# Kernel tuning notes

Hardware: AMD Instinct MI355X
Metric: run time of the kernel (lower is better)

Reference implementation:

```python
import jax, jax.numpy as jnp
import numpy as np

RETURN_SHAPE = (128, 128)


def dht2(x):
    # Discrete Hartley Transform over the spatial axes (2, 3):
    # H = Re(FFT) - Im(FFT). Unnormalized, matching scipy.fft default.
    f = jnp.fft.fftn(x, axes=(2, 3))
    return f.real - f.imag


def setup_inputs() -> dict:
    key = jax.random.key(0)
    x = jax.random.normal(key, (8, 64, 256, 256), dtype=jnp.float32)
    return {"x": x}


def reference(x) -> jnp.ndarray:
    # Spectral pooling: DHT -> center crop in frequency domain -> DHT.
    h_out, w_out = RETURN_SHAPE
    H, W = x.shape[2], x.shape[3]
    d = dht2(x)
    sh = (H - h_out) // 2
    sw = (W - w_out) // 2
    cropped = d[:, :, sh:sh + h_out, sw:sw + w_out]
    return dht2(cropped).astype(jnp.float32)
```

## Files before the change

kernel.cpp:

```cpp
#include <hip/hip_runtime.h>
#include <math.h>


typedef __attribute__((ext_vector_type(8))) short bfrag;
typedef __attribute__((ext_vector_type(4))) float ffrag;

#define PI2_256 0.0245436926061702597f
#define PI2_128 0.0490873852123405194f

__device__ __forceinline__ unsigned short f2bf(float f) {
    union { float f; unsigned int u; } v; v.f = f;
    unsigned int r = v.u + 0x7fffu + ((v.u >> 16) & 1u);
    return (unsigned short)(r >> 16);
}

__device__ __forceinline__ bfrag pack8(float4 a, float4 b) {
    bfrag r;
    r[0] = (short)f2bf(a.x); r[1] = (short)f2bf(a.y);
    r[2] = (short)f2bf(a.z); r[3] = (short)f2bf(a.w);
    r[4] = (short)f2bf(b.x); r[5] = (short)f2bf(b.y);
    r[6] = (short)f2bf(b.z); r[7] = (short)f2bf(b.w);
    return r;
}

__global__ __launch_bounds__(256) void gen_tables(unsigned short* __restrict__ ws)
{
    const int id = blockIdx.x * 256 + threadIdx.x;
    {
        const int u = id >> 9, k = id & 511;
        const int up = 64 + u;
        float s, c, val;
        if (k < 256) { sincosf((float)((up * k) & 255) * PI2_256, &s, &c); val = c; }
        else         { sincosf((float)((up * (k - 256)) & 255) * PI2_256, &s, &c); val = s; }
        ws[36864 + id] = f2bf(val);
    }
    if (id < 36864) {
        const int c = id >> 8, m = id & 255;
        const int idx = ((64 + c) * m) & 255;
        float s, cc; sincosf((float)idx * PI2_256, &s, &cc);
        ws[id] = f2bf(cc + s);
    }
    if (id < 16384) {
        const int c = id >> 7, m = id & 127;
        const int idx = (c * m) & 127;
        float s, cc; sincosf((float)idx * PI2_128, &s, &cc);
        ws[102400 + id] = f2bf(cc + s);
    }
    if (id < 32768) {
        const int u = id >> 8, k = id & 255;
        float s, c, val;
        if (k < 128) { sincosf((float)((u * k) & 127) * PI2_128, &s, &c); val = c; }
        else         { sincosf((float)((u * (k - 128)) & 127) * PI2_128, &s, &c); val = s; }
        ws[118784 + id] = f2bf(val);
    }
}

__global__ __launch_bounds__(512, 4) void stage1(const float* __restrict__ X,
                                                 const unsigned short* __restrict__ ws,
                                                 float* __restrict__ dc)
{
    __shared__ unsigned short Pt[129 * 256];

    const int t  = threadIdx.x;
    const int w  = t >> 6;
    const int ln = t & 15;
    const int q  = (t & 63) >> 4;

    const float* __restrict__ Xi = X + (size_t)blockIdx.x * 65536;
    const unsigned short* __restrict__ W1 = ws;
    const unsigned short* __restrict__ W2 = ws + 36864;

#pragma unroll
    for (int rp = 0; rp < 2; ++rp) {
        const int base = rp * 128 + w * 16;
        ffrag acc[9];
#pragma unroll
        for (int nt = 0; nt < 9; ++nt) acc[nt] = (ffrag){0.f, 0.f, 0.f, 0.f};

        const float* __restrict__ xrow = Xi + (size_t)(base + ln) * 256;
#pragma unroll
        for (int kk = 0; kk < 8; ++kk) {
            const int k = kk * 32 + q * 8;
            const float4 x0 = *(const float4*)(xrow + k);
            const float4 x1 = *(const float4*)(xrow + k + 4);
            const bfrag A = pack8(x0, x1);
#pragma unroll
            for (int nt = 0; nt < 9; ++nt) {
                const bfrag B = *(const bfrag*)(W1 + (nt * 16 + ln) * 256 + k);
                acc[nt] = __builtin_amdgcn_mfma_f32_16x16x32_bf16(A, B, acc[nt], 0, 0, 0);
            }
        }
        const int n0 = base + 4 * q;
#pragma unroll
        for (int nt = 0; nt < 9; ++nt) {
            const int c = nt * 16 + ln;
            if (nt < 8 || ln == 0) {
                const unsigned int lo = (unsigned int)f2bf(acc[nt][0]) |
                                        ((unsigned int)f2bf(acc[nt][1]) << 16);
                const unsigned int hi = (unsigned int)f2bf(acc[nt][2]) |
                                        ((unsigned int)f2bf(acc[nt][3]) << 16);
                const int phys = c * 256 + (((n0 >> 3) ^ (c & 7)) << 3) + (n0 & 7);
                *(uint2*)&Pt[phys] = make_uint2(lo, hi);
            }
        }
    }
    __syncthreads();

    {
        ffrag acc[8];
#pragma unroll
        for (int nt = 0; nt < 8; ++nt) acc[nt] = (ffrag){0.f, 0.f, 0.f, 0.f};

        const int u0 = w * 16;
#pragma unroll
        for (int kk = 0; kk < 16; ++kk) {
            const int k = kk * 32 + q * 8;
            const bfrag A = *(const bfrag*)(W2 + (size_t)(u0 + ln) * 512 + k);
            const bool loK = (kk < 8);
#pragma unroll
            for (int nt = 0; nt < 8; ++nt) {
                const int v   = nt * 16 + ln;
                const int row = loK ? v : (128 - v);
                const int col = loK ? k : (k - 256);
                const int phys = row * 256 + (((col >> 3) ^ (row & 7)) << 3);
                const bfrag B = *(const bfrag*)&Pt[phys];
                acc[nt] = __builtin_amdgcn_mfma_f32_16x16x32_bf16(A, B, acc[nt], 0, 0, 0);
            }
        }
        float* __restrict__ D = dc + (size_t)blockIdx.x * 16384;
#pragma unroll
        for (int nt = 0; nt < 8; ++nt) {
#pragma unroll
            for (int r = 0; r < 4; ++r) {
                D[(u0 + 4 * q + r) * 128 + nt * 16 + ln] = acc[nt][r];
            }
        }
    }
}

__global__ __launch_bounds__(512, 4) void stage2(const unsigned short* __restrict__ ws,
                                                 float* __restrict__ io)
{
    __shared__ unsigned short P2t[128 * 128];

    const int t  = threadIdx.x;
    const int w  = t >> 6;
    const int ln = t & 15;
    const int q  = (t & 63) >> 4;

    float* __restrict__ G = io + (size_t)blockIdx.x * 16384;
    const unsigned short* __restrict__ W3 = ws + 102400;
    const unsigned short* __restrict__ W4 = ws + 118784;

    {
        ffrag acc[8];
#pragma unroll
        for (int nt = 0; nt < 8; ++nt) acc[nt] = (ffrag){0.f, 0.f, 0.f, 0.f};

        const int p0 = w * 16;
        const float* __restrict__ drow = G + (size_t)(p0 + ln) * 128;
#pragma unroll
        for (int kk = 0; kk < 4; ++kk) {
            const int k = kk * 32 + q * 8;
            const float4 x0 = *(const float4*)(drow + k);
            const float4 x1 = *(const float4*)(drow + k + 4);
            const bfrag A = pack8(x0, x1);
#pragma unroll
            for (int nt = 0; nt < 8; ++nt) {
                const bfrag B = *(const bfrag*)(W3 + (nt * 16 + ln) * 128 + k);
                acc[nt] = __builtin_amdgcn_mfma_f32_16x16x32_bf16(A, B, acc[nt], 0, 0, 0);
            }
        }
        const int n0 = p0 + 4 * q;
#pragma unroll
        for (int nt = 0; nt < 8; ++nt) {
            const int c = nt * 16 + ln;
            const unsigned int lo = (unsigned int)f2bf(acc[nt][0]) |
                                    ((unsigned int)f2bf(acc[nt][1]) << 16);
            const unsigned int hi = (unsigned int)f2bf(acc[nt][2]) |
                                    ((unsigned int)f2bf(acc[nt][3]) << 16);
            const int phys = c * 128 + (((n0 >> 3) ^ (c & 7)) << 3) + (n0 & 7);
            *(uint2*)&P2t[phys] = make_uint2(lo, hi);
        }
    }
    __syncthreads();

    {
        ffrag o[8];
#pragma unroll
        for (int nt = 0; nt < 8; ++nt) o[nt] = (ffrag){0.f, 0.f, 0.f, 0.f};

        const int u0 = w * 16;
#pragma unroll
        for (int kk = 0; kk < 8; ++kk) {
            const int k = kk * 32 + q * 8;
            const bfrag A = *(const bfrag*)(W4 + (size_t)(u0 + ln) * 256 + k);
            const bool loK = (kk < 4);
#pragma unroll
            for (int nt = 0; nt < 8; ++nt) {
                const int v   = nt * 16 + ln;
                const int row = loK ? v : ((128 - v) & 127);
                const int col = loK ? k : (k - 128);
                const int phys = row * 128 + (((col >> 3) ^ (row & 7)) << 3);
                const bfrag B = *(const bfrag*)&P2t[phys];
                o[nt] = __builtin_amdgcn_mfma_f32_16x16x32_bf16(A, B, o[nt], 0, 0, 0);
            }
        }
#pragma unroll
        for (int nt = 0; nt < 8; ++nt) {
#pragma unroll
            for (int r = 0; r < 4; ++r) {
                G[(u0 + 4 * q + r) * 128 + nt * 16 + ln] = o[nt][r];
            }
        }
    }
}

extern "C" void kernel_launch(void* const* d_in, const int* in_sizes, int n_in,
                              void* d_out, int out_size, void* d_ws, size_t ws_size,
                              hipStream_t stream)
{
    const float* x = (const float*)d_in[0];
    float* out = (float*)d_out;
    unsigned short* tw = (unsigned short*)d_ws;

    gen_tables<<<dim3(256), dim3(256), 0, stream>>>(tw);
    stage1<<<dim3(512), dim3(512), 0, stream>>>(x, tw, out);
    stage2<<<dim3(512), dim3(512), 0, stream>>>(tw, out);
}
```

Measured before the change: 299.7 us.

## Fuse both DHT stages into one 1024-thread kernel with LDS-staged I/O

Merges stage1 and stage2 into a single kernel so the intermediate 128x128 cropped spectrum stays in shared memory as bf16 instead of round-tripping through global memory. Input rows are loaded with coalesced float4 reads, converted to bf16 and staged in padded LDS, with the second half prefetched into registers while the first half is computed. Output goes through LDS for coalesced float4 stores. Work is split across 16 waves, and the XOR swizzle is replaced by row padding. In exchange it uses much more LDS (about 135 KB per block), which limits occupancy, and adds extra bf16 rounding of the intermediate.

```diff
diff --git a/kernel.cpp b/kernel.cpp
--- a/kernel.cpp
+++ b/kernel.cpp
@@ -7,6 +7,11 @@
 
 #define PI2_256 0.0245436926061702597f
 #define PI2_128 0.0490873852123405194f
+
+constexpr int PT_E  = 0;
+constexpr int XB_E  = 34056;
+constexpr int DCB_E = 34056;
+constexpr int P2T_E = 51464;
 
 __device__ __forceinline__ unsigned short f2bf(float f) {
     union { float f; unsigned int u; } v; v.f = f;
@@ -14,12 +19,10 @@
     return (unsigned short)(r >> 16);
 }
 
-__device__ __forceinline__ bfrag pack8(float4 a, float4 b) {
-    bfrag r;
-    r[0] = (short)f2bf(a.x); r[1] = (short)f2bf(a.y);
-    r[2] = (short)f2bf(a.z); r[3] = (short)f2bf(a.w);
-    r[4] = (short)f2bf(b.x); r[5] = (short)f2bf(b.y);
-    r[6] = (short)f2bf(b.z); r[7] = (short)f2bf(b.w);
+__device__ __forceinline__ uint2 pack4(float4 a) {
+    uint2 r;
+    r.x = (unsigned)f2bf(a.x) | ((unsigned)f2bf(a.y) << 16);
+    r.y = (unsigned)f2bf(a.z) | ((unsigned)f2bf(a.w) << 16);
     return r;
 }
 
@@ -36,14 +39,12 @@
     }
     if (id < 36864) {
         const int c = id >> 8, m = id & 255;
-        const int idx = ((64 + c) * m) & 255;
-        float s, cc; sincosf((float)idx * PI2_256, &s, &cc);
+        float s, cc; sincosf((float)(((64 + c) * m) & 255) * PI2_256, &s, &cc);
         ws[id] = f2bf(cc + s);
     }
     if (id < 16384) {
         const int c = id >> 7, m = id & 127;
-        const int idx = (c * m) & 127;
-        float s, cc; sincosf((float)idx * PI2_128, &s, &cc);
+        float s, cc; sincosf((float)((c * m) & 127) * PI2_128, &s, &cc);
         ws[102400 + id] = f2bf(cc + s);
     }
     if (id < 32768) {
@@ -55,163 +56,182 @@
     }
 }
 
-__global__ __launch_bounds__(512, 4) void stage1(const float* __restrict__ X,
+__device__ __forceinline__ void phaseA(unsigned short* sm, const unsigned short* W1,
+                                       int pan, int w, int ln, int q)
+{
+    const int a   = w & 7;
+    const int ct0 = (w >> 3) * 4;
+    ffrag acc[5];
+#pragma unroll
+    for (int i = 0; i < 5; ++i) acc[i] = (ffrag){0.f, 0.f, 0.f, 0.f};
+
+#pragma unroll
+    for (int kk = 0; kk < 8; ++kk) {
+        const int k = kk * 32 + q * 8;
+        const bfrag A = *(const bfrag*)&sm[XB_E + (a * 16 + ln) * 264 + k];
+#pragma unroll
+        for (int i = 0; i < 5; ++i) {
+            const bfrag B = *(const bfrag*)(W1 + ((ct0 + i) * 16 + ln) * 256 + k);
+            acc[i] = __builtin_amdgcn_mfma_f32_16x16x32_bf16(A, B, acc[i], 0, 0, 0);
+        }
+    }
+    const int nb = pan * 128 + a * 16 + 4 * q;
+#pragma unroll
+    for (int i = 0; i < 5; ++i) {
+        const int cc = (ct0 + i) * 16 + ln;
+        if (cc <= 128) {
+            uint2 vv;
+            vv.x = (unsigned)f2bf(acc[i][0]) | ((unsigned)f2bf(acc[i][1]) << 16);
+            vv.y = (unsigned)f2bf(acc[i][2]) | ((unsigned)f2bf(acc[i][3]) << 16);
+            *(uint2*)&sm[PT_E + cc * 264 + nb] = vv;
+        }
+    }
+}
+
+__global__ __launch_bounds__(1024, 4) void fused(const float* __restrict__ X,
                                                  const unsigned short* __restrict__ ws,
-                                                 float* __restrict__ dc)
-{
-    __shared__ unsigned short Pt[129 * 256];
+                                                 float* __restrict__ out)
+{
+    __shared__ unsigned short sm[68872];
+    float* outS = (float*)sm;
 
     const int t  = threadIdx.x;
     const int w  = t >> 6;
     const int ln = t & 15;
     const int q  = (t & 63) >> 4;
-
     const float* __restrict__ Xi = X + (size_t)blockIdx.x * 65536;
+
     const unsigned short* __restrict__ W1 = ws;
     const unsigned short* __restrict__ W2 = ws + 36864;
-
-#pragma unroll
-    for (int rp = 0; rp < 2; ++rp) {
-        const int base = rp * 128 + w * 16;
-        ffrag acc[9];
-#pragma unroll
-        for (int nt = 0; nt < 9; ++nt) acc[nt] = (ffrag){0.f, 0.f, 0.f, 0.f};
-
-        const float* __restrict__ xrow = Xi + (size_t)(base + ln) * 256;
-#pragma unroll
-        for (int kk = 0; kk < 8; ++kk) {
-            const int k = kk * 32 + q * 8;
-            const float4 x0 = *(const float4*)(xrow + k);
-            const float4 x1 = *(const float4*)(xrow + k + 4);
-            const bfrag A = pack8(x0, x1);
-#pragma unroll
-            for (int nt = 0; nt < 9; ++nt) {
-                const bfrag B = *(const bfrag*)(W1 + (nt * 16 + ln) * 256 + k);
-                acc[nt] = __builtin_amdgcn_mfma_f32_16x16x32_bf16(A, B, acc[nt], 0, 0, 0);
-            }
-        }
-        const int n0 = base + 4 * q;
-#pragma unroll
-        for (int nt = 0; nt < 9; ++nt) {
-            const int c = nt * 16 + ln;
-            if (nt < 8 || ln == 0) {
-                const unsigned int lo = (unsigned int)f2bf(acc[nt][0]) |
-                                        ((unsigned int)f2bf(acc[nt][1]) << 16);
-                const unsigned int hi = (unsigned int)f2bf(acc[nt][2]) |
-                                        ((unsigned int)f2bf(acc[nt][3]) << 16);
-                const int phys = c * 256 + (((n0 >> 3) ^ (c & 7)) << 3) + (n0 & 7);
-                *(uint2*)&Pt[phys] = make_uint2(lo, hi);
-            }
-        }
-    }
-    __syncthreads();
-
-    {
-        ffrag acc[8];
-#pragma unroll
-        for (int nt = 0; nt < 8; ++nt) acc[nt] = (ffrag){0.f, 0.f, 0.f, 0.f};
-
-        const int u0 = w * 16;
+    const unsigned short* __restrict__ W3 = ws + 102400;
+    const unsigned short* __restrict__ W4 = ws + 118784;
+
+    float4 r0[8], r1[8];
+#pragma unroll
+    for (int i = 0; i < 8; ++i) r0[i] = ((const float4*)Xi)[i * 1024 + t];
+#pragma unroll
+    for (int i = 0; i < 8; ++i) {
+        const int f = i * 1024 + t;
+        const int n = f >> 6, m = (f & 63) * 4;
+        *(uint2*)&sm[XB_E + n * 264 + m] = pack4(r0[i]);
+    }
+    __syncthreads();
+
+#pragma unroll
+    for (int i = 0; i < 8; ++i) r1[i] = ((const float4*)(Xi + 32768))[i * 1024 + t];
+
+    phaseA(sm, W1, 0, w, ln, q);
+    __syncthreads();
+
+#pragma unroll
+    for (int i = 0; i < 8; ++i) {
+        const int f = i * 1024 + t;
+        const int n = f >> 6, m = (f & 63) * 4;
+        *(uint2*)&sm[XB_E + n * 264 + m] = pack4(r1[i]);
+    }
+    __syncthreads();
+
+    phaseA(sm, W1, 1, w, ln, q);
+    __syncthreads();
+
+    {
+        const int u0 = (w & 7) * 16;
+        const int vh = w >> 3;
+        ffrag acc[4];
+#pragma unroll
+        for (int i = 0; i < 4; ++i) acc[i] = (ffrag){0.f, 0.f, 0.f, 0.f};
+
 #pragma unroll
         for (int kk = 0; kk < 16; ++kk) {
             const int k = kk * 32 + q * 8;
             const bfrag A = *(const bfrag*)(W2 + (size_t)(u0 + ln) * 512 + k);
             const bool loK = (kk < 8);
 #pragma unroll
-            for (int nt = 0; nt < 8; ++nt) {
-                const int v   = nt * 16 + ln;
+            for (int i = 0; i < 4; ++i) {
+                const int v   = (vh * 4 + i) * 16 + ln;
                 const int row = loK ? v : (128 - v);
                 const int col = loK ? k : (k - 256);
-                const int phys = row * 256 + (((col >> 3) ^ (row & 7)) << 3);
-                const bfrag B = *(const bfrag*)&Pt[phys];
-                acc[nt] = __builtin_amdgcn_mfma_f32_16x16x32_bf16(A, B, acc[nt], 0, 0, 0);
+                const bfrag B = *(const bfrag*)&sm[PT_E + row * 264 + col];
+                acc[i] = __builtin_amdgcn_mfma_f32_16x16x32_bf16(A, B, acc[i], 0, 0, 0);
             }
         }
-        float* __restrict__ D = dc + (size_t)blockIdx.x * 16384;
-#pragma unroll
-        for (int nt = 0; nt < 8; ++nt) {
-#pragma unroll
-            for (int r = 0; r < 4; ++r) {
-                D[(u0 + 4 * q + r) * 128 + nt * 16 + ln] = acc[nt][r];
-            }
-        }
-    }
-}
-
-__global__ __launch_bounds__(512, 4) void stage2(const unsigned short* __restrict__ ws,
-                                                 float* __restrict__ io)
-{
-    __shared__ unsigned short P2t[128 * 128];
-
-    const int t  = threadIdx.x;
-    const int w  = t >> 6;
-    const int ln = t & 15;
-    const int q  = (t & 63) >> 4;
-
-    float* __restrict__ G = io + (size_t)blockIdx.x * 16384;
-    const unsigned short* __restrict__ W3 = ws + 102400;
-    const unsigned short* __restrict__ W4 = ws + 118784;
-
-    {
-        ffrag acc[8];
-#pragma unroll
-        for (int nt = 0; nt < 8; ++nt) acc[nt] = (ffrag){0.f, 0.f, 0.f, 0.f};
-
-        const int p0 = w * 16;
-        const float* __restrict__ drow = G + (size_t)(p0 + ln) * 128;
+#pragma unroll
+        for (int i = 0; i < 4; ++i) {
+            const int v = (vh * 4 + i) * 16 + ln;
+#pragma unroll
+            for (int r = 0; r < 4; ++r)
+                sm[DCB_E + (u0 + 4 * q + r) * 136 + v] = f2bf(acc[i][r]);
+        }
+    }
+    __syncthreads();
+
+    {
+        const int p0  = (w & 7) * 16;
+        const int ct0 = (w >> 3) * 4;
+        ffrag acc[4];
+#pragma unroll
+        for (int i = 0; i < 4; ++i) acc[i] = (ffrag){0.f, 0.f, 0.f, 0.f};
+
 #pragma unroll
         for (int kk = 0; kk < 4; ++kk) {
             const int k = kk * 32 + q * 8;
-            const float4 x0 = *(const float4*)(drow + k);
-            const float4 x1 = *(const float4*)(drow + k + 4);
-            const bfrag A = pack8(x0, x1);
-#pragma unroll
-            for (int nt = 0; nt < 8; ++nt) {
-                const bfrag B = *(const bfrag*)(W3 + (nt * 16 + ln) * 128 + k);
-                acc[nt] = __builtin_amdgcn_mfma_f32_16x16x32_bf16(A, B, acc[nt], 0, 0, 0);
+            const bfrag A = *(const bfrag*)&sm[DCB_E + (p0 + ln) * 136 + k];
+#pragma unroll
+            for (int i = 0; i < 4; ++i) {
+                const bfrag B = *(const bfrag*)(W3 + ((ct0 + i) * 16 + ln) * 128 + k);
+                acc[i] = __builtin_amdgcn_mfma_f32_16x16x32_bf16(A, B, acc[i], 0, 0, 0);
             }
         }
-        const int n0 = p0 + 4 * q;
-#pragma unroll
-        for (int nt = 0; nt < 8; ++nt) {
-            const int c = nt * 16 + ln;
-            const unsigned int lo = (unsigned int)f2bf(acc[nt][0]) |
-                                    ((unsigned int)f2bf(acc[nt][1]) << 16);
-            const unsigned int hi = (unsigned int)f2bf(acc[nt][2]) |
-                                    ((unsigned int)f2bf(acc[nt][3]) << 16);
-            const int phys = c * 128 + (((n0 >> 3) ^ (c & 7)) << 3) + (n0 & 7);
-            *(uint2*)&P2t[phys] = make_uint2(lo, hi);
-        }
-    }
-    __syncthreads();
-
-    {
-        ffrag o[8];
-#pragma unroll
-        for (int nt = 0; nt < 8; ++nt) o[nt] = (ffrag){0.f, 0.f, 0.f, 0.f};
-
-        const int u0 = w * 16;
+#pragma unroll
+        for (int i = 0; i < 4; ++i) {
+            const int cc = (ct0 + i) * 16 + ln;
+            uint2 vv;
+            vv.x = (unsigned)f2bf(acc[i][0]) | ((unsigned)f2bf(acc[i][1]) << 16);
+            vv.y = (unsigned)f2bf(acc[i][2]) | ((unsigned)f2bf(acc[i][3]) << 16);
+            *(uint2*)&sm[P2T_E + cc * 136 + p0 + 4 * q] = vv;
+        }
+    }
+    __syncthreads();
+
+    {
+        const int u0 = (w & 7) * 16;
+        const int vh = w >> 3;
+        ffrag o[4];
+#pragma unroll
+        for (int i = 0; i < 4; ++i) o[i] = (ffrag){0.f, 0.f, 0.f, 0.f};
+
 #pragma unroll
         for (int kk = 0; kk < 8; ++kk) {
             const int k = kk * 32 + q * 8;
             const bfrag A = *(const bfrag*)(W4 + (size_t)(u0 + ln) * 256 + k);
             const bool loK = (kk < 4);
 #pragma unroll
-            for (int nt = 0; nt < 8; ++nt) {
-                const int v   = nt * 16 + ln;
+            for (int i = 0; i < 4; ++i) {
+                const int v   = (vh * 4 + i) * 16 + ln;
                 const int row = loK ? v : ((128 - v) & 127);
                 const int col = loK ? k : (k - 128);
-                const int phys = row * 128 + (((col >> 3) ^ (row & 7)) << 3);
-                const bfrag B = *(const bfrag*)&P2t[phys];
-                o[nt] = __builtin_amdgcn_mfma_f32_16x16x32_bf16(A, B, o[nt], 0, 0, 0);
+                const bfrag B = *(const bfrag*)&sm[P2T_E + row * 136 + col];
+                o[i] = __builtin_amdgcn_mfma_f32_16x16x32_bf16(A, B, o[i], 0, 0, 0);
             }
         }
 #pragma unroll
-        for (int nt = 0; nt < 8; ++nt) {
-#pragma unroll
-            for (int r = 0; r < 4; ++r) {
-                G[(u0 + 4 * q + r) * 128 + nt * 16 + ln] = o[nt][r];
-            }
+        for (int i = 0; i < 4; ++i) {
+            const int v = (vh * 4 + i) * 16 + ln;
+#pragma unroll
+            for (int r = 0; r < 4; ++r)
+                outS[(u0 + 4 * q + r) * 132 + v] = o[i][r];
+        }
+    }
+    __syncthreads();
+
+    {
+        float* __restrict__ G = out + (size_t)blockIdx.x * 16384;
+#pragma unroll
+        for (int i = 0; i < 4; ++i) {
+            const int f  = i * 1024 + t;
+            const int u  = f >> 5, v4 = f & 31;
+            const float4 val = *(const float4*)&outS[u * 132 + v4 * 4];
+            *(float4*)&G[u * 128 + v4 * 4] = val;
         }
     }
 }
@@ -225,6 +245,5 @@
     unsigned short* tw = (unsigned short*)d_ws;
 
     gen_tables<<<dim3(256), dim3(256), 0, stream>>>(tw);
-    stage1<<<dim3(512), dim3(512), 0, stream>>>(x, tw, out);
-    stage2<<<dim3(512), dim3(512), 0, stream>>>(tw, out);
-}
+    fused<<<dim3(512), dim3(1024), 0, stream>>>(x, tw, out);
+}
```

Measured after the change: 292.8 us. 1.02x faster.

## Fuse both DHT stages into one kernel keeping intermediate in LDS

Applied to the files above, without the earlier changes.

Merges stage1 and stage2 into a single kernel, so the cropped 128x128 intermediate stays in shared memory as bf16 instead of being written to and re-read from global memory as fp32. LDS layouts switch from XOR swizzle to padded row strides. The final output is staged through LDS in two passes so it can be written with coalesced float4 stores. This saves a kernel launch and a global round trip, but adds extra barriers and an extra bf16 rounding of the intermediate.

```diff
diff --git a/kernel.cpp b/kernel.cpp
--- a/kernel.cpp
+++ b/kernel.cpp
@@ -7,6 +7,11 @@
 
 #define PI2_256 0.0245436926061702597f
 #define PI2_128 0.0490873852123405194f
+
+constexpr int PT_S   = 264;
+constexpr int DCB_E  = 0;
+constexpr int P2T_E  = 17408;
+constexpr int SM_EL  = 34816;
 
 __device__ __forceinline__ unsigned short f2bf(float f) {
     union { float f; unsigned int u; } v; v.f = f;
@@ -23,6 +28,13 @@
     return r;
 }
 
+__device__ __forceinline__ uint2 packacc(ffrag a) {
+    uint2 r;
+    r.x = (unsigned)f2bf(a[0]) | ((unsigned)f2bf(a[1]) << 16);
+    r.y = (unsigned)f2bf(a[2]) | ((unsigned)f2bf(a[3]) << 16);
+    return r;
+}
+
 __global__ __launch_bounds__(256) void gen_tables(unsigned short* __restrict__ ws)
 {
     const int id = blockIdx.x * 256 + threadIdx.x;
@@ -36,14 +48,12 @@
     }
     if (id < 36864) {
         const int c = id >> 8, m = id & 255;
-        const int idx = ((64 + c) * m) & 255;
-        float s, cc; sincosf((float)idx * PI2_256, &s, &cc);
+        float s, cc; sincosf((float)(((64 + c) * m) & 255) * PI2_256, &s, &cc);
         ws[id] = f2bf(cc + s);
     }
     if (id < 16384) {
         const int c = id >> 7, m = id & 127;
-        const int idx = (c * m) & 127;
-        float s, cc; sincosf((float)idx * PI2_128, &s, &cc);
+        float s, cc; sincosf((float)((c * m) & 127) * PI2_128, &s, &cc);
         ws[102400 + id] = f2bf(cc + s);
     }
     if (id < 32768) {
@@ -55,11 +65,12 @@
     }
 }
 
-__global__ __launch_bounds__(512, 4) void stage1(const float* __restrict__ X,
-                                                 const unsigned short* __restrict__ ws,
-                                                 float* __restrict__ dc)
+__global__ __launch_bounds__(512, 4) void fused(const float* __restrict__ X,
+                                                const unsigned short* __restrict__ ws,
+                                                float* __restrict__ out)
 {
-    __shared__ unsigned short Pt[129 * 256];
+    __shared__ unsigned short sm[SM_EL];
+    float* outS = (float*)sm;
 
     const int t  = threadIdx.x;
     const int w  = t >> 6;
@@ -69,149 +80,136 @@
     const float* __restrict__ Xi = X + (size_t)blockIdx.x * 65536;
     const unsigned short* __restrict__ W1 = ws;
     const unsigned short* __restrict__ W2 = ws + 36864;
-
-#pragma unroll
-    for (int rp = 0; rp < 2; ++rp) {
-        const int base = rp * 128 + w * 16;
+    const unsigned short* __restrict__ W3 = ws + 102400;
+    const unsigned short* __restrict__ W4 = ws + 118784;
+
+#pragma unroll
+    for (int half = 0; half < 2; ++half) {
+        const int n0 = w * 32 + half * 16;
         ffrag acc[9];
 #pragma unroll
-        for (int nt = 0; nt < 9; ++nt) acc[nt] = (ffrag){0.f, 0.f, 0.f, 0.f};
-
-        const float* __restrict__ xrow = Xi + (size_t)(base + ln) * 256;
+        for (int i = 0; i < 9; ++i) acc[i] = (ffrag){0.f, 0.f, 0.f, 0.f};
+
+        const float* __restrict__ xrow = Xi + (size_t)(n0 + ln) * 256;
 #pragma unroll
         for (int kk = 0; kk < 8; ++kk) {
             const int k = kk * 32 + q * 8;
-            const float4 x0 = *(const float4*)(xrow + k);
-            const float4 x1 = *(const float4*)(xrow + k + 4);
-            const bfrag A = pack8(x0, x1);
-#pragma unroll
-            for (int nt = 0; nt < 9; ++nt) {
-                const bfrag B = *(const bfrag*)(W1 + (nt * 16 + ln) * 256 + k);
-                acc[nt] = __builtin_amdgcn_mfma_f32_16x16x32_bf16(A, B, acc[nt], 0, 0, 0);
-            }
-        }
-        const int n0 = base + 4 * q;
-#pragma unroll
-        for (int nt = 0; nt < 9; ++nt) {
-            const int c = nt * 16 + ln;
-            if (nt < 8 || ln == 0) {
-                const unsigned int lo = (unsigned int)f2bf(acc[nt][0]) |
-                                        ((unsigned int)f2bf(acc[nt][1]) << 16);
-                const unsigned int hi = (unsigned int)f2bf(acc[nt][2]) |
-                                        ((unsigned int)f2bf(acc[nt][3]) << 16);
-                const int phys = c * 256 + (((n0 >> 3) ^ (c & 7)) << 3) + (n0 & 7);
-                *(uint2*)&Pt[phys] = make_uint2(lo, hi);
-            }
+            const bfrag A = pack8(*(const float4*)(xrow + k),
+                                  *(const float4*)(xrow + k + 4));
+#pragma unroll
+            for (int ct = 0; ct < 9; ++ct) {
+                const bfrag B = *(const bfrag*)(W1 + (ct * 16 + ln) * 256 + k);
+                acc[ct] = __builtin_amdgcn_mfma_f32_16x16x32_bf16(A, B, acc[ct], 0, 0, 0);
+            }
+        }
+        const int nb = n0 + 4 * q;
+#pragma unroll
+        for (int ct = 0; ct < 9; ++ct) {
+            const int cc = ct * 16 + ln;
+            if (cc <= 128)
+                *(uint2*)&sm[cc * PT_S + nb] = packacc(acc[ct]);
         }
     }
     __syncthreads();
 
     {
+        const int u0 = w * 16;
         ffrag acc[8];
 #pragma unroll
-        for (int nt = 0; nt < 8; ++nt) acc[nt] = (ffrag){0.f, 0.f, 0.f, 0.f};
-
-        const int u0 = w * 16;
+        for (int i = 0; i < 8; ++i) acc[i] = (ffrag){0.f, 0.f, 0.f, 0.f};
+
 #pragma unroll
         for (int kk = 0; kk < 16; ++kk) {
             const int k = kk * 32 + q * 8;
             const bfrag A = *(const bfrag*)(W2 + (size_t)(u0 + ln) * 512 + k);
-            const bool loK = (kk < 8);
+            const bool lo = (kk < 8);
 #pragma unroll
             for (int nt = 0; nt < 8; ++nt) {
                 const int v   = nt * 16 + ln;
-                const int row = loK ? v : (128 - v);
-                const int col = loK ? k : (k - 256);
-                const int phys = row * 256 + (((col >> 3) ^ (row & 7)) << 3);
-                const bfrag B = *(const bfrag*)&Pt[phys];
+                const int row = lo ? v : (128 - v);
+                const int col = lo ? k : (k - 256);
+                const bfrag B = *(const bfrag*)&sm[row * PT_S + col];
                 acc[nt] = __builtin_amdgcn_mfma_f32_16x16x32_bf16(A, B, acc[nt], 0, 0, 0);
             }
         }
-        float* __restrict__ D = dc + (size_t)blockIdx.x * 16384;
+        __syncthreads();
 #pragma unroll
         for (int nt = 0; nt < 8; ++nt) {
-#pragma unroll
-            for (int r = 0; r < 4; ++r) {
-                D[(u0 + 4 * q + r) * 128 + nt * 16 + ln] = acc[nt][r];
-            }
-        }
-    }
-}
-
-__global__ __launch_bounds__(512, 4) void stage2(const unsigned short* __restrict__ ws,
-                                                 float* __restrict__ io)
-{
-    __shared__ unsigned short P2t[128 * 128];
-
-    const int t  = threadIdx.x;
-    const int w  = t >> 6;
-    const int ln = t & 15;
-    const int q  = (t & 63) >> 4;
-
-    float* __restrict__ G = io + (size_t)blockIdx.x * 16384;
-    const unsigned short* __restrict__ W3 = ws + 102400;
-    const unsigned short* __restrict__ W4 = ws + 118784;
-
-    {
+            const int v = nt * 16 + ln;
+#pragma unroll
+            for (int r = 0; r < 4; ++r)
+                sm[DCB_E + (u0 + 4 * q + r) * 136 + v] = f2bf(acc[nt][r]);
+        }
+    }
+    __syncthreads();
+
+    {
+        const int p0 = w * 16;
         ffrag acc[8];
 #pragma unroll
-        for (int nt = 0; nt < 8; ++nt) acc[nt] = (ffrag){0.f, 0.f, 0.f, 0.f};
-
-        const int p0 = w * 16;
-        const float* __restrict__ drow = G + (size_t)(p0 + ln) * 128;
+        for (int i = 0; i < 8; ++i) acc[i] = (ffrag){0.f, 0.f, 0.f, 0.f};
+
 #pragma unroll
         for (int kk = 0; kk < 4; ++kk) {
             const int k = kk * 32 + q * 8;
-            const float4 x0 = *(const float4*)(drow + k);
-            const float4 x1 = *(const float4*)(drow + k + 4);
-            const bfrag A = pack8(x0, x1);
-#pragma unroll
-            for (int nt = 0; nt < 8; ++nt) {
-                const bfrag B = *(const bfrag*)(W3 + (nt * 16 + ln) * 128 + k);
-                acc[nt] = __builtin_amdgcn_mfma_f32_16x16x32_bf16(A, B, acc[nt], 0, 0, 0);
-            }
-        }
-        const int n0 = p0 + 4 * q;
-#pragma unroll
-        for (int nt = 0; nt < 8; ++nt) {
-            const int c = nt * 16 + ln;
-            const unsigned int lo = (unsigned int)f2bf(acc[nt][0]) |
-                                    ((unsigned int)f2bf(acc[nt][1]) << 16);
-            const unsigned int hi = (unsigned int)f2bf(acc[nt][2]) |
-                                    ((unsigned int)f2bf(acc[nt][3]) << 16);
-            const int phys = c * 128 + (((n0 >> 3) ^ (c & 7)) << 3) + (n0 & 7);
-            *(uint2*)&P2t[phys] = make_uint2(lo, hi);
+            const bfrag A = *(const bfrag*)&sm[DCB_E + (p0 + ln) * 136 + k];
+#pragma unroll
+            for (int ct = 0; ct < 8; ++ct) {
+                const bfrag B = *(const bfrag*)(W3 + (ct * 16 + ln) * 128 + k);
+                acc[ct] = __builtin_amdgcn_mfma_f32_16x16x32_bf16(A, B, acc[ct], 0, 0, 0);
+            }
+        }
+#pragma unroll
+        for (int ct = 0; ct < 8; ++ct) {
+            const int cc = ct * 16 + ln;
+            *(uint2*)&sm[P2T_E + cc * 136 + p0 + 4 * q] = packacc(acc[ct]);
         }
     }
     __syncthreads();
 
     {
+        const int u0 = w * 16;
         ffrag o[8];
 #pragma unroll
-        for (int nt = 0; nt < 8; ++nt) o[nt] = (ffrag){0.f, 0.f, 0.f, 0.f};
-
-        const int u0 = w * 16;
+        for (int i = 0; i < 8; ++i) o[i] = (ffrag){0.f, 0.f, 0.f, 0.f};
+
 #pragma unroll
         for (int kk = 0; kk < 8; ++kk) {
             const int k = kk * 32 + q * 8;
             const bfrag A = *(const bfrag*)(W4 + (size_t)(u0 + ln) * 256 + k);
-            const bool loK = (kk < 4);
+            const bool lo = (kk < 4);
 #pragma unroll
             for (int nt = 0; nt < 8; ++nt) {
                 const int v   = nt * 16 + ln;
-                const int row = loK ? v : ((128 - v) & 127);
-                const int col = loK ? k : (k - 128);
-                const int phys = row * 128 + (((col >> 3) ^ (row & 7)) << 3);
-                const bfrag B = *(const bfrag*)&P2t[phys];
+                const int row = lo ? v : ((128 - v) & 127);
+                const int col = lo ? k : (k - 128);
+                const bfrag B = *(const bfrag*)&sm[P2T_E + row * 136 + col];
                 o[nt] = __builtin_amdgcn_mfma_f32_16x16x32_bf16(A, B, o[nt], 0, 0, 0);
             }
         }
-#pragma unroll
-        for (int nt = 0; nt < 8; ++nt) {
-#pragma unroll
-            for (int r = 0; r < 4; ++r) {
-                G[(u0 + 4 * q + r) * 128 + nt * 16 + ln] = o[nt][r];
-            }
+
+        float* __restrict__ G = out + (size_t)blockIdx.x * 16384;
+#pragma unroll
+        for (int pass = 0; pass < 2; ++pass) {
+            if ((w >> 2) == pass) {
+                const int ul0 = (w & 3) * 16;
+#pragma unroll
+                for (int nt = 0; nt < 8; ++nt) {
+                    const int v = nt * 16 + ln;
+#pragma unroll
+                    for (int r = 0; r < 4; ++r)
+                        outS[(ul0 + 4 * q + r) * 132 + v] = o[nt][r];
+                }
+            }
+            __syncthreads();
+#pragma unroll
+            for (int i = 0; i < 4; ++i) {
+                const int f = i * 512 + t;
+                const int u = f >> 5, v4 = f & 31;
+                *(float4*)&G[(pass * 64 + u) * 128 + v4 * 4] =
+                    *(const float4*)&outS[u * 132 + v4 * 4];
+            }
+            __syncthreads();
         }
     }
 }
@@ -225,6 +223,5 @@
     unsigned short* tw = (unsigned short*)d_ws;
 
     gen_tables<<<dim3(256), dim3(256), 0, stream>>>(tw);
-    stage1<<<dim3(512), dim3(512), 0, stream>>>(x, tw, out);
-    stage2<<<dim3(512), dim3(512), 0, stream>>>(tw, out);
-}
+    fused<<<dim3(512), dim3(512), 0, stream>>>(x, tw, out);
+}
```

Result: no change. 302.5 us (+0.9%).
